# Kernel tuning notes

Measured on AMD Instinct MI355X. Metric: run time of the kernel, lower is better.

## Reference

```python
import jax, jax.numpy as jnp
import numpy as np

K = 8
HID = 32
BOUND = 5.0
SIGMA_MIN = 1e-4
MIN_DERIV = 1e-3
B, T, C = 32, 4096, 512


def setup_inputs() -> dict:
    key = jax.random.key(0)
    k1, k2, k3 = jax.random.split(key, 3)
    x = jax.random.normal(k1, (B, T, C), jnp.float32)
    W1 = jax.random.normal(k2, (HID, 2), jnp.float32) * 0.5
    b1 = jnp.zeros((HID,), jnp.float32)
    W2 = jax.random.normal(k3, (3 * K + 1, HID), jnp.float32) * 0.1
    b2 = jnp.zeros((3 * K + 1,), jnp.float32)
    return {"x": x, "W1": W1, "b1": b1, "W2": W2, "b2": b2}


def _rqs_forward(x2d, kx, ky, d):
    # x2d: (BC, T); kx, ky, d: (BC, K+1)
    w = kx[:, 1:] - kx[:, :-1]
    h = ky[:, 1:] - ky[:, :-1]
    s = h / jnp.maximum(w, 1e-8)
    idx = jax.vmap(lambda a, v: jnp.searchsorted(a, v, side='right'))(kx, x2d) - 1
    idx = jnp.clip(idx, 0, K - 1)  # (BC, T)
    g = lambda t, i: jnp.take_along_axis(t, i, axis=1)
    w_k = g(w, idx)
    h_k = g(h, idx)
    s_k = g(s, idx)
    d_k = g(d, idx)
    d_k1 = g(d, jnp.minimum(idx + 1, K))
    kx_l = g(kx, idx)
    ky_l = g(ky, idx)
    zeta = jnp.clip((x2d - kx_l) / jnp.maximum(w_k, 1e-8), 0.0, 1.0)
    numer = h_k * (s_k * zeta * zeta + d_k * zeta * (1.0 - zeta))
    denom = s_k + (d_k1 + d_k - 2.0 * s_k) * zeta * (1.0 - zeta)
    z2d = ky_l + numer / jnp.maximum(denom, 1e-8)
    tail = (x2d < -BOUND) | (x2d > BOUND)
    return jnp.where(tail, x2d, z2d)


def reference(x, W1, b1, W2, b2):
    Bb, Tt, Cc = x.shape
    # affine standardisation (unbiased std matching torch.std default)
    mu = jnp.mean(x, axis=1, keepdims=True)
    sig = jnp.maximum(jnp.std(x, axis=1, ddof=1, keepdims=True), SIGMA_MIN)
    z_pre = (x - mu) / sig  # (B, T, C)
    zd = jax.lax.stop_gradient(z_pre)
    skew = jnp.mean(zd ** 3, axis=1)          # (B, C)
    ekurt = jnp.mean(zd ** 4, axis=1) - 3.0   # (B, C)
    stats = jnp.stack([skew, ekurt], axis=-1).reshape(Bb * Cc, 2)
    hid = jax.nn.relu(stats @ W1.T + b1)
    raw = hid @ W2.T + b2                      # (BC, 3K+1)
    widths = jax.nn.softmax(raw[:, :K], axis=-1) * (2.0 * BOUND)
    heights = jax.nn.softmax(raw[:, K:2 * K], axis=-1) * (2.0 * BOUND)
    derivs = jax.nn.softplus(raw[:, 2 * K:]) + MIN_DERIV  # (BC, K+1)
    pad = jnp.full((widths.shape[0], 1), -BOUND, widths.dtype)
    kx = jnp.concatenate([pad, -BOUND + jnp.cumsum(widths, axis=-1)], axis=-1)
    ky = jnp.concatenate([pad, -BOUND + jnp.cumsum(heights, axis=-1)], axis=-1)
    x2d = jnp.transpose(z_pre, (0, 2, 1)).reshape(Bb * Cc, Tt)
    z2d = _rqs_forward(x2d, kx, ky, derivs)
    return jnp.transpose(z2d.reshape(Bb, Cc, Tt), (0, 2, 1))
```

## Files before the change

### kernel.cpp

```cpp
#include <hip/hip_runtime.h>
#include <math.h>

#define KNOTS 8
#define HIDN 32
#define TT 4096
#define CC 512
#define NB 32
#define BOUNDF 5.0f
#define CT 32
#define NTG 64
#define NLD 64
#define NPAIR 128
#define TPAD 9

typedef float f32x4 __attribute__((ext_vector_type(4)));

__global__ __launch_bounds__(512, 2)
void k_fused(const float* __restrict__ x, const float* __restrict__ W1,
             const float* __restrict__ b1, const float* __restrict__ W2,
             const float* __restrict__ b2, float* __restrict__ out)
{
    const int bb = blockIdx.y;
    const int c0 = blockIdx.x * CT;
    const int lc = threadIdx.x & 7;
    const int tg = threadIdx.x >> 3;

    __shared__ float red[NTG][4][CT];
    __shared__ float mom[4][CT];
    __shared__ float pA[CT], pB[CT];
    __shared__ float pKx[7][CT];
    __shared__ float2 bZ4[4][KNOTS][TPAD];
    __shared__ float2 bY4[4][KNOTS][TPAD];
    __shared__ float2 bD4[4][KNOTS][TPAD];

    const size_t base = (size_t)bb * TT * CC + c0 + 4 * lc + (size_t)tg * CC;
    const f32x4* pxt = (const f32x4*)(x + base);

    unsigned int xp[NPAIR];
    float s1[4] = {0,0,0,0}, s2[4] = {0,0,0,0}, s3[4] = {0,0,0,0}, s4[4] = {0,0,0,0};
    #pragma unroll
    for (int k = 0; k < NLD; ++k) {
        const f32x4 v = pxt[(size_t)k * (NTG * CC / 4)];
        #pragma unroll
        for (int q = 0; q < 4; ++q) {
            const float vv = v[q];
            const float v2 = vv * vv;
            s1[q] += vv;
            s2[q] = fmaf(vv, vv, s2[q]);
            s3[q] = fmaf(v2, vv, s3[q]);
            s4[q] = fmaf(v2, v2, s4[q]);
        }
        unsigned int pk0, pk1;
        asm("v_cvt_pk_bf16_f32 %0, %1, %2" : "=v"(pk0) : "v"(v[0]), "v"(v[1]));
        asm("v_cvt_pk_bf16_f32 %0, %1, %2" : "=v"(pk1) : "v"(v[2]), "v"(v[3]));
        xp[2*k]   = pk0;
        xp[2*k+1] = pk1;
    }
    #pragma unroll
    for (int q = 0; q < 4; ++q) {
        red[tg][0][4*lc+q] = s1[q];
        red[tg][1][4*lc+q] = s2[q];
        red[tg][2][4*lc+q] = s3[q];
        red[tg][3][4*lc+q] = s4[q];
    }
    __syncthreads();

    if (threadIdx.x < 4 * CT) {
        const int m = threadIdx.x >> 5, c = threadIdx.x & (CT - 1);
        float acc = 0.f;
        #pragma unroll
        for (int g = 0; g < NTG; ++g) acc += red[g][m][c];
        mom[m][c] = acc;
    }
    __syncthreads();

    if (threadIdx.x < CT) {
        const int c = threadIdx.x;
        const float n  = (float)TT;
        const float t1 = mom[0][c], t2 = mom[1][c], t3 = mom[2][c], t4 = mom[3][c];
        const float mu  = t1 / n;
        const float ex2 = t2 / n, ex3 = t3 / n, ex4 = t4 / n;
        float var = (t2 - n * mu * mu) / (n - 1.f);
        var = fmaxf(var, 0.f);
        const float sig  = fmaxf(sqrtf(var), 1e-4f);
        const float inv  = 1.f / sig;
        const float mu2  = mu * mu;
        const float ez3  = ex3 - 3.f * mu * ex2 + 2.f * mu * mu2;
        const float ez4  = ex4 - 4.f * mu * ex3 + 6.f * mu2 * ex2 - 3.f * mu2 * mu2;
        const float inv2 = inv * inv;
        const float skew  = ez3 * inv2 * inv;
        const float ekurt = ez4 * inv2 * inv2 - 3.f;

        float hid[HIDN];
        #pragma unroll
        for (int h = 0; h < HIDN; ++h) {
            float v = fmaf(W1[2*h], skew, fmaf(W1[2*h+1], ekurt, b1[h]));
            hid[h] = fmaxf(v, 0.f);
        }

        float e[KNOTS], kxr[KNOTS+1], kyr[KNOTS+1], dr[KNOTS+1];
        {
            float mx = -1e30f;
            #pragma unroll
            for (int o = 0; o < KNOTS; ++o) {
                float acc = b2[o];
                #pragma unroll
                for (int h = 0; h < HIDN; ++h) acc = fmaf(W2[o*HIDN + h], hid[h], acc);
                e[o] = acc; mx = fmaxf(mx, acc);
            }
            float sum = 0.f;
            #pragma unroll
            for (int o = 0; o < KNOTS; ++o) { e[o] = expf(e[o] - mx); sum += e[o]; }
            const float scale = (2.f * BOUNDF) / sum;
            float cum = -BOUNDF; kxr[0] = -BOUNDF;
            #pragma unroll
            for (int o = 0; o < KNOTS; ++o) { cum = fmaf(e[o], scale, cum); kxr[o+1] = cum; }
        }
        {
            float mx = -1e30f;
            #pragma unroll
            for (int o = 0; o < KNOTS; ++o) {
                float acc = b2[KNOTS + o];
                #pragma unroll
                for (int h = 0; h < HIDN; ++h) acc = fmaf(W2[(KNOTS+o)*HIDN + h], hid[h], acc);
                e[o] = acc; mx = fmaxf(mx, acc);
            }
            float sum = 0.f;
            #pragma unroll
            for (int o = 0; o < KNOTS; ++o) { e[o] = expf(e[o] - mx); sum += e[o]; }
            const float scale = (2.f * BOUNDF) / sum;
            float cum = -BOUNDF; kyr[0] = -BOUNDF;
            #pragma unroll
            for (int o = 0; o < KNOTS; ++o) { cum = fmaf(e[o], scale, cum); kyr[o+1] = cum; }
        }
        #pragma unroll
        for (int o = 0; o < KNOTS+1; ++o) {
            float acc = b2[2*KNOTS + o];
            #pragma unroll
            for (int h = 0; h < HIDN; ++h) acc = fmaf(W2[(2*KNOTS+o)*HIDN + h], hid[h], acc);
            float sp = fmaxf(acc, 0.f) + log1pf(expf(-fabsf(acc)));
            dr[o] = sp + 1e-3f;
        }

        pA[c] = inv;
        pB[c] = -mu * inv;
        #pragma unroll
        for (int j = 1; j <= 7; ++j) pKx[j-1][c] = kxr[j];
        const int q = c & 3, cc = c >> 2;
        #pragma unroll
        for (int j = 0; j < KNOTS; ++j) {
            const float w    = kxr[j+1] - kxr[j];
            const float wm   = fmaxf(w, 1e-8f);
            const float invw = 1.f / wm;
            const float h    = kyr[j+1] - kyr[j];
            bZ4[q][j][cc] = make_float2(-kxr[j] * invw, invw);
            bY4[q][j][cc] = make_float2(kyr[j], h);
            bD4[q][j][cc] = make_float2(dr[j], dr[j] + dr[j+1]);
        }
    }
    __syncthreads();

    float aq[4], bq[4], kx[4][7];
    #pragma unroll
    for (int q = 0; q < 4; ++q) {
        const int c = 4*lc + q;
        aq[q] = pA[c];
        bq[q] = pB[c];
        #pragma unroll
        for (int j = 0; j < 7; ++j) kx[q][j] = pKx[j][c];
    }
    f32x4* pot = (f32x4*)(out + base);

    #pragma unroll
    for (int k = 0; k < NLD; ++k) {
        const unsigned int u0 = xp[2*k], u1 = xp[2*k+1];
        float xv[4];
        xv[0] = __uint_as_float(u0 << 16);
        xv[1] = __uint_as_float(u0 & 0xffff0000u);
        xv[2] = __uint_as_float(u1 << 16);
        xv[3] = __uint_as_float(u1 & 0xffff0000u);
        f32x4 r;
        #pragma unroll
        for (int q = 0; q < 4; ++q) {
            const float z = fmaf(xv[q], aq[q], bq[q]);
            const bool  c4 = z >= kx[q][3];
            const float mB = c4 ? kx[q][5] : kx[q][1];
            const bool  cB = z >= mB;
            const float nLo = c4 ? kx[q][4] : kx[q][0];
            const float nHi = c4 ? kx[q][6] : kx[q][2];
            const float mC = cB ? nHi : nLo;
            const bool  cC = z >= mC;
            const int idx = (c4 ? 4 : 0) + (cB ? 2 : 0) + (cC ? 1 : 0);

            const float2 Z = bZ4[q][idx][lc];
            const float2 Y = bY4[q][idx][lc];
            const float2 D = bD4[q][idx][lc];

            const float zeta = fmaf(z, Z.y, Z.x);
            const float uu   = fmaf(-zeta, zeta, zeta);
            const float s    = Y.y * Z.y;
            const float R    = fmaf(-2.f, s, D.y);
            const float den  = fmaf(R, uu, s);
            const float inner= fmaf(s * zeta, zeta, D.x * uu);
            const float res  = fmaf(Y.y * inner,
                                    __builtin_amdgcn_rcpf(fmaxf(den, 1e-8f)), Y.x);
            r[q] = (fabsf(z) > BOUNDF) ? z : res;
        }
        __builtin_nontemporal_store(r, &pot[(size_t)k * (NTG * CC / 4)]);
    }
}

extern "C" void kernel_launch(void* const* d_in, const int* in_sizes, int n_in,
                              void* d_out, int out_size, void* d_ws, size_t ws_size,
                              hipStream_t stream) {
    const float* x  = (const float*)d_in[0];
    const float* W1 = (const float*)d_in[1];
    const float* b1 = (const float*)d_in[2];
    const float* W2 = (const float*)d_in[3];
    const float* b2 = (const float*)d_in[4];
    float* out = (float*)d_out;

    k_fused<<<dim3(CC / CT, NB), dim3(512), 0, stream>>>(x, W1, b1, W2, b2, out);
}
```

Baseline: 120.2 us.

## Split fused kernel into stats and apply kernels with workspace parameter tiles

Splits the single fused kernel into a statistics kernel that computes moments and spline parameters into a global workspace, and an apply kernel that re-reads x from memory. This removes the bf16 register cache of x and the register pressure that limited occupancy, and adds more parallelism in the apply phase. In exchange it reads the input twice from global memory and adds a second launch. The stats reduction also moves to wave shuffles.

```diff
diff --git a/kernel.cpp b/kernel.cpp
--- a/kernel.cpp
+++ b/kernel.cpp
@@ -7,74 +7,78 @@
 #define CC 512
 #define NB 32
 #define BOUNDF 5.0f
-#define CT 32
-#define NTG 64
-#define NLD 64
-#define NPAIR 128
-#define TPAD 9
+
+#define BZOFF 288
+#define BYOFF 1344
+#define BDOFF 2400
+#define TILEF 3456
 
 typedef float f32x4 __attribute__((ext_vector_type(4)));
 
-__global__ __launch_bounds__(512, 2)
-void k_fused(const float* __restrict__ x, const float* __restrict__ W1,
+__global__ __launch_bounds__(1024, 4)
+void k_stats(const float* __restrict__ x, const float* __restrict__ W1,
              const float* __restrict__ b1, const float* __restrict__ W2,
-             const float* __restrict__ b2, float* __restrict__ out)
+             const float* __restrict__ b2, float* __restrict__ ws)
 {
     const int bb = blockIdx.y;
-    const int c0 = blockIdx.x * CT;
+    const int ctile = blockIdx.x;
+    const int c0 = ctile * 32;
     const int lc = threadIdx.x & 7;
     const int tg = threadIdx.x >> 3;
-
-    __shared__ float red[NTG][4][CT];
-    __shared__ float mom[4][CT];
-    __shared__ float pA[CT], pB[CT];
-    __shared__ float pKx[7][CT];
-    __shared__ float2 bZ4[4][KNOTS][TPAD];
-    __shared__ float2 bY4[4][KNOTS][TPAD];
-    __shared__ float2 bD4[4][KNOTS][TPAD];
-
-    const size_t base = (size_t)bb * TT * CC + c0 + 4 * lc + (size_t)tg * CC;
-    const f32x4* pxt = (const f32x4*)(x + base);
-
-    unsigned int xp[NPAIR];
+    const int w  = threadIdx.x >> 6;
+    const int ln = threadIdx.x & 63;
+
+    __shared__ float red4[16][4][32];
+    __shared__ float mom[4][32];
+
+    const f32x4* pxt = (const f32x4*)(x + (size_t)bb * TT * CC + c0 + 4 * lc
+                                        + (size_t)tg * CC);
+    const size_t stride4 = (size_t)128 * CC / 4;
+
     float s1[4] = {0,0,0,0}, s2[4] = {0,0,0,0}, s3[4] = {0,0,0,0}, s4[4] = {0,0,0,0};
     #pragma unroll
-    for (int k = 0; k < NLD; ++k) {
-        const f32x4 v = pxt[(size_t)k * (NTG * CC / 4)];
-        #pragma unroll
-        for (int q = 0; q < 4; ++q) {
-            const float vv = v[q];
-            const float v2 = vv * vv;
+    for (int k = 0; k < 32; ++k) {
+        const f32x4 v = pxt[(size_t)k * stride4];
+        #pragma unroll
+        for (int q = 0; q < 4; ++q) {
+            const float vv = v[q], v2 = vv * vv;
             s1[q] += vv;
             s2[q] = fmaf(vv, vv, s2[q]);
             s3[q] = fmaf(v2, vv, s3[q]);
             s4[q] = fmaf(v2, v2, s4[q]);
         }
-        unsigned int pk0, pk1;
-        asm("v_cvt_pk_bf16_f32 %0, %1, %2" : "=v"(pk0) : "v"(v[0]), "v"(v[1]));
-        asm("v_cvt_pk_bf16_f32 %0, %1, %2" : "=v"(pk1) : "v"(v[2]), "v"(v[3]));
-        xp[2*k]   = pk0;
-        xp[2*k+1] = pk1;
     }
     #pragma unroll
-    for (int q = 0; q < 4; ++q) {
-        red[tg][0][4*lc+q] = s1[q];
-        red[tg][1][4*lc+q] = s2[q];
-        red[tg][2][4*lc+q] = s3[q];
-        red[tg][3][4*lc+q] = s4[q];
+    for (int m = 8; m < 64; m <<= 1) {
+        #pragma unroll
+        for (int q = 0; q < 4; ++q) {
+            s1[q] += __shfl_xor(s1[q], m, 64);
+            s2[q] += __shfl_xor(s2[q], m, 64);
+            s3[q] += __shfl_xor(s3[q], m, 64);
+            s4[q] += __shfl_xor(s4[q], m, 64);
+        }
+    }
+    if (ln < 8) {
+        #pragma unroll
+        for (int q = 0; q < 4; ++q) {
+            red4[w][0][4*ln+q] = s1[q];
+            red4[w][1][4*ln+q] = s2[q];
+            red4[w][2][4*ln+q] = s3[q];
+            red4[w][3][4*ln+q] = s4[q];
+        }
     }
     __syncthreads();
 
-    if (threadIdx.x < 4 * CT) {
-        const int m = threadIdx.x >> 5, c = threadIdx.x & (CT - 1);
+    if (threadIdx.x < 128) {
+        const int m = threadIdx.x >> 5, c = threadIdx.x & 31;
         float acc = 0.f;
         #pragma unroll
-        for (int g = 0; g < NTG; ++g) acc += red[g][m][c];
+        for (int g = 0; g < 16; ++g) acc += red4[g][m][c];
         mom[m][c] = acc;
     }
     __syncthreads();
 
-    if (threadIdx.x < CT) {
+    if (threadIdx.x < 32) {
         const int c = threadIdx.x;
         const float n  = (float)TT;
         const float t1 = mom[0][c], t2 = mom[1][c], t3 = mom[2][c], t4 = mom[3][c];
@@ -142,21 +146,43 @@
             dr[o] = sp + 1e-3f;
         }
 
-        pA[c] = inv;
-        pB[c] = -mu * inv;
-        #pragma unroll
-        for (int j = 1; j <= 7; ++j) pKx[j-1][c] = kxr[j];
-        const int q = c & 3, cc = c >> 2;
+        float* tb = ws + (size_t)(bb * 16 + ctile) * TILEF;
+        tb[c]      = inv;
+        tb[32 + c] = -mu * inv;
+        #pragma unroll
+        for (int j = 1; j <= 7; ++j) tb[64 + (j-1)*32 + c] = kxr[j];
+        float2* bz = (float2*)(tb + BZOFF);
+        float2* by = (float2*)(tb + BYOFF);
+        float2* bd = (float2*)(tb + BDOFF);
         #pragma unroll
         for (int j = 0; j < KNOTS; ++j) {
-            const float w    = kxr[j+1] - kxr[j];
-            const float wm   = fmaxf(w, 1e-8f);
+            const float wd   = kxr[j+1] - kxr[j];
+            const float wm   = fmaxf(wd, 1e-8f);
             const float invw = 1.f / wm;
             const float h    = kyr[j+1] - kyr[j];
-            bZ4[q][j][cc] = make_float2(-kxr[j] * invw, invw);
-            bY4[q][j][cc] = make_float2(kyr[j], h);
-            bD4[q][j][cc] = make_float2(dr[j], dr[j] + dr[j+1]);
-        }
+            bz[j*33 + c] = make_float2(-kxr[j] * invw, invw);
+            by[j*33 + c] = make_float2(kyr[j], h);
+            bd[j*33 + c] = make_float2(dr[j], dr[j] + dr[j+1]);
+        }
+    }
+}
+
+__global__ __launch_bounds__(256, 6)
+void k_apply(const float* __restrict__ x, const float* __restrict__ ws,
+             float* __restrict__ out)
+{
+    const int tch   = blockIdx.x;
+    const int ctile = blockIdx.y;
+    const int bb    = blockIdx.z;
+    const int c0 = ctile * 32;
+    const int lc = threadIdx.x & 7;
+    const int tg = threadIdx.x >> 3;
+
+    __shared__ float sp[TILEF];
+    {
+        const f32x4* src = (const f32x4*)(ws + (size_t)(bb * 16 + ctile) * TILEF);
+        f32x4* dst = (f32x4*)sp;
+        for (int i = threadIdx.x; i < TILEF / 4; i += 256) dst[i] = src[i];
     }
     __syncthreads();
 
@@ -164,25 +190,28 @@
     #pragma unroll
     for (int q = 0; q < 4; ++q) {
         const int c = 4*lc + q;
-        aq[q] = pA[c];
-        bq[q] = pB[c];
-        #pragma unroll
-        for (int j = 0; j < 7; ++j) kx[q][j] = pKx[j][c];
-    }
-    f32x4* pot = (f32x4*)(out + base);
-
-    #pragma unroll
-    for (int k = 0; k < NLD; ++k) {
-        const unsigned int u0 = xp[2*k], u1 = xp[2*k+1];
-        float xv[4];
-        xv[0] = __uint_as_float(u0 << 16);
-        xv[1] = __uint_as_float(u0 & 0xffff0000u);
-        xv[2] = __uint_as_float(u1 << 16);
-        xv[3] = __uint_as_float(u1 & 0xffff0000u);
+        aq[q] = sp[c];
+        bq[q] = sp[32 + c];
+        #pragma unroll
+        for (int j = 0; j < 7; ++j) kx[q][j] = sp[64 + j*32 + c];
+    }
+    const float2* bz = (const float2*)(sp + BZOFF);
+    const float2* by = (const float2*)(sp + BYOFF);
+    const float2* bd = (const float2*)(sp + BDOFF);
+
+    const size_t base = (size_t)bb * TT * CC + (size_t)(tch * 512 + tg) * CC
+                        + c0 + 4 * lc;
+    const f32x4* pxt = (const f32x4*)(x + base);
+    f32x4*       pot = (f32x4*)(out + base);
+    const size_t stride4 = (size_t)32 * CC / 4;
+
+    #pragma unroll 4
+    for (int k = 0; k < 16; ++k) {
+        const f32x4 v = pxt[(size_t)k * stride4];
         f32x4 r;
         #pragma unroll
         for (int q = 0; q < 4; ++q) {
-            const float z = fmaf(xv[q], aq[q], bq[q]);
+            const float z = fmaf(v[q], aq[q], bq[q]);
             const bool  c4 = z >= kx[q][3];
             const float mB = c4 ? kx[q][5] : kx[q][1];
             const bool  cB = z >= mB;
@@ -191,10 +220,11 @@
             const float mC = cB ? nHi : nLo;
             const bool  cC = z >= mC;
             const int idx = (c4 ? 4 : 0) + (cB ? 2 : 0) + (cC ? 1 : 0);
-
-            const float2 Z = bZ4[q][idx][lc];
-            const float2 Y = bY4[q][idx][lc];
-            const float2 D = bD4[q][idx][lc];
+            const int off = idx * 33 + 4*lc + q;
+
+            const float2 Z = bz[off];
+            const float2 Y = by[off];
+            const float2 D = bd[off];
 
             const float zeta = fmaf(z, Z.y, Z.x);
             const float uu   = fmaf(-zeta, zeta, zeta);
@@ -206,7 +236,7 @@
                                     __builtin_amdgcn_rcpf(fmaxf(den, 1e-8f)), Y.x);
             r[q] = (fabsf(z) > BOUNDF) ? z : res;
         }
-        __builtin_nontemporal_store(r, &pot[(size_t)k * (NTG * CC / 4)]);
+        __builtin_nontemporal_store(r, &pot[(size_t)k * stride4]);
     }
 }
 
@@ -219,6 +249,8 @@
     const float* W2 = (const float*)d_in[3];
     const float* b2 = (const float*)d_in[4];
     float* out = (float*)d_out;
-
-    k_fused<<<dim3(CC / CT, NB), dim3(512), 0, stream>>>(x, W1, b1, W2, b2, out);
+    float* ws  = (float*)d_ws;
+
+    k_stats<<<dim3(16, NB), dim3(1024), 0, stream>>>(x, W1, b1, W2, b2, ws);
+    k_apply<<<dim3(8, 16, NB), dim3(256), 0, stream>>>(x, ws, out);
 }
```

Result: slower. 156.0 us (+29.8%).

## Process two channel tiles per block, overlapping second tile's loads with first tile's stores

Applied to the files above, without the earlier changes.

Each block now handles 64 channels as two 32-channel tiles. While the transform of tile A runs and its results are stored, the loads and moment accumulation for tile B happen in the same loop, so load and store traffic overlap. The per-channel moment reduction also moves from a 64-row shared-memory table to wave-level shuffle reductions plus a small 8-row table. The cost is half as many blocks (256 instead of 512), which may reduce occupancy and latency hiding across the GPU, and a serial finalize phase between the tiles.

```diff
diff --git a/kernel.cpp b/kernel.cpp
--- a/kernel.cpp
+++ b/kernel.cpp
@@ -7,13 +7,98 @@
 #define CC 512
 #define NB 32
 #define BOUNDF 5.0f
-#define CT 32
-#define NTG 64
 #define NLD 64
-#define NPAIR 128
-#define TPAD 9
+#define TPAD 33
 
 typedef float f32x4 __attribute__((ext_vector_type(4)));
+
+__device__ __forceinline__ void finalize_ch(
+    int c, float t1, float t2, float t3, float t4,
+    const float* __restrict__ W1, const float* __restrict__ b1,
+    const float* __restrict__ W2, const float* __restrict__ b2,
+    float* pA, float* pB, float* pKx ,
+    float2* bz, float2* by, float2* bd )
+{
+    const float n  = (float)TT;
+    const float mu  = t1 / n;
+    const float ex2 = t2 / n, ex3 = t3 / n, ex4 = t4 / n;
+    float var = (t2 - n * mu * mu) / (n - 1.f);
+    var = fmaxf(var, 0.f);
+    const float sig  = fmaxf(sqrtf(var), 1e-4f);
+    const float inv  = 1.f / sig;
+    const float mu2  = mu * mu;
+    const float ez3  = ex3 - 3.f * mu * ex2 + 2.f * mu * mu2;
+    const float ez4  = ex4 - 4.f * mu * ex3 + 6.f * mu2 * ex2 - 3.f * mu2 * mu2;
+    const float inv2 = inv * inv;
+    const float skew  = ez3 * inv2 * inv;
+    const float ekurt = ez4 * inv2 * inv2 - 3.f;
+
+    float hid[HIDN];
+    #pragma unroll
+    for (int h = 0; h < HIDN; ++h) {
+        float v = fmaf(W1[2*h], skew, fmaf(W1[2*h+1], ekurt, b1[h]));
+        hid[h] = fmaxf(v, 0.f);
+    }
+
+    float e[KNOTS], kxr[KNOTS+1], kyr[KNOTS+1], dr[KNOTS+1];
+    {
+        float mx = -1e30f;
+        #pragma unroll
+        for (int o = 0; o < KNOTS; ++o) {
+            float acc = b2[o];
+            #pragma unroll
+            for (int h = 0; h < HIDN; ++h) acc = fmaf(W2[o*HIDN + h], hid[h], acc);
+            e[o] = acc; mx = fmaxf(mx, acc);
+        }
+        float sum = 0.f;
+        #pragma unroll
+        for (int o = 0; o < KNOTS; ++o) { e[o] = expf(e[o] - mx); sum += e[o]; }
+        const float scale = (2.f * BOUNDF) / sum;
+        float cum = -BOUNDF; kxr[0] = -BOUNDF;
+        #pragma unroll
+        for (int o = 0; o < KNOTS; ++o) { cum = fmaf(e[o], scale, cum); kxr[o+1] = cum; }
+    }
+    {
+        float mx = -1e30f;
+        #pragma unroll
+        for (int o = 0; o < KNOTS; ++o) {
+            float acc = b2[KNOTS + o];
+            #pragma unroll
+            for (int h = 0; h < HIDN; ++h) acc = fmaf(W2[(KNOTS+o)*HIDN + h], hid[h], acc);
+            e[o] = acc; mx = fmaxf(mx, acc);
+        }
+        float sum = 0.f;
+        #pragma unroll
+        for (int o = 0; o < KNOTS; ++o) { e[o] = expf(e[o] - mx); sum += e[o]; }
+        const float scale = (2.f * BOUNDF) / sum;
+        float cum = -BOUNDF; kyr[0] = -BOUNDF;
+        #pragma unroll
+        for (int o = 0; o < KNOTS; ++o) { cum = fmaf(e[o], scale, cum); kyr[o+1] = cum; }
+    }
+    #pragma unroll
+    for (int o = 0; o < KNOTS+1; ++o) {
+        float acc = b2[2*KNOTS + o];
+        #pragma unroll
+        for (int h = 0; h < HIDN; ++h) acc = fmaf(W2[(2*KNOTS+o)*HIDN + h], hid[h], acc);
+        float sp = fmaxf(acc, 0.f) + log1pf(expf(-fabsf(acc)));
+        dr[o] = sp + 1e-3f;
+    }
+
+    pA[c] = inv;
+    pB[c] = -mu * inv;
+    #pragma unroll
+    for (int j = 1; j <= 7; ++j) pKx[(j-1)*32 + c] = kxr[j];
+    #pragma unroll
+    for (int j = 0; j < KNOTS; ++j) {
+        const float wd   = kxr[j+1] - kxr[j];
+        const float wm   = fmaxf(wd, 1e-8f);
+        const float invw = 1.f / wm;
+        const float h    = kyr[j+1] - kyr[j];
+        bz[j*TPAD + c] = make_float2(-kxr[j] * invw, invw);
+        by[j*TPAD + c] = make_float2(kyr[j], h);
+        bd[j*TPAD + c] = make_float2(dr[j], dr[j] + dr[j+1]);
+    }
+}
 
 __global__ __launch_bounds__(512, 2)
 void k_fused(const float* __restrict__ x, const float* __restrict__ W1,
@@ -21,30 +106,34 @@
              const float* __restrict__ b2, float* __restrict__ out)
 {
     const int bb = blockIdx.y;
-    const int c0 = blockIdx.x * CT;
+    const int jj = blockIdx.x;
+    const int c0a = jj * 64;
     const int lc = threadIdx.x & 7;
     const int tg = threadIdx.x >> 3;
-
-    __shared__ float red[NTG][4][CT];
-    __shared__ float mom[4][CT];
-    __shared__ float pA[CT], pB[CT];
-    __shared__ float pKx[7][CT];
-    __shared__ float2 bZ4[4][KNOTS][TPAD];
-    __shared__ float2 bY4[4][KNOTS][TPAD];
-    __shared__ float2 bD4[4][KNOTS][TPAD];
-
-    const size_t base = (size_t)bb * TT * CC + c0 + 4 * lc + (size_t)tg * CC;
-    const f32x4* pxt = (const f32x4*)(x + base);
-
-    unsigned int xp[NPAIR];
+    const int w  = threadIdx.x >> 6;
+    const int ln = threadIdx.x & 63;
+
+    __shared__ float red4[8][4][32];
+    __shared__ float mom[4][32];
+    __shared__ float pA[2][32], pB[2][32], pKx[2][7*32];
+    __shared__ float2 bzT[2][KNOTS*TPAD], byT[2][KNOTS*TPAD], bdT[2][KNOTS*TPAD];
+
+    const size_t baseA = (size_t)bb * TT * CC + c0a + 4 * lc + (size_t)tg * CC;
+    const f32x4* pxA = (const f32x4*)(x + baseA);
+    const f32x4* pxB = (const f32x4*)(x + baseA + 32);
+    f32x4* poA = (f32x4*)(out + baseA);
+    f32x4* poB = (f32x4*)(out + baseA + 32);
+    const size_t stride4 = (size_t)64 * CC / 4;
+
+    unsigned int xp[2 * NLD];
     float s1[4] = {0,0,0,0}, s2[4] = {0,0,0,0}, s3[4] = {0,0,0,0}, s4[4] = {0,0,0,0};
+
     #pragma unroll
     for (int k = 0; k < NLD; ++k) {
-        const f32x4 v = pxt[(size_t)k * (NTG * CC / 4)];
-        #pragma unroll
-        for (int q = 0; q < 4; ++q) {
-            const float vv = v[q];
-            const float v2 = vv * vv;
+        const f32x4 v = pxA[(size_t)k * stride4];
+        #pragma unroll
+        for (int q = 0; q < 4; ++q) {
+            const float vv = v[q], v2 = vv * vv;
             s1[q] += vv;
             s2[q] = fmaf(vv, vv, s2[q]);
             s3[q] = fmaf(v2, vv, s3[q]);
@@ -53,123 +142,145 @@
         unsigned int pk0, pk1;
         asm("v_cvt_pk_bf16_f32 %0, %1, %2" : "=v"(pk0) : "v"(v[0]), "v"(v[1]));
         asm("v_cvt_pk_bf16_f32 %0, %1, %2" : "=v"(pk1) : "v"(v[2]), "v"(v[3]));
-        xp[2*k]   = pk0;
-        xp[2*k+1] = pk1;
-    }
-    #pragma unroll
-    for (int q = 0; q < 4; ++q) {
-        red[tg][0][4*lc+q] = s1[q];
-        red[tg][1][4*lc+q] = s2[q];
-        red[tg][2][4*lc+q] = s3[q];
-        red[tg][3][4*lc+q] = s4[q];
-    }
-    __syncthreads();
-
-    if (threadIdx.x < 4 * CT) {
-        const int m = threadIdx.x >> 5, c = threadIdx.x & (CT - 1);
+        xp[2*k] = pk0; xp[2*k+1] = pk1;
+    }
+    #pragma unroll
+    for (int m = 8; m < 64; m <<= 1)
+        #pragma unroll
+        for (int q = 0; q < 4; ++q) {
+            s1[q] += __shfl_xor(s1[q], m, 64);
+            s2[q] += __shfl_xor(s2[q], m, 64);
+            s3[q] += __shfl_xor(s3[q], m, 64);
+            s4[q] += __shfl_xor(s4[q], m, 64);
+        }
+    if (ln < 8) {
+        #pragma unroll
+        for (int q = 0; q < 4; ++q) {
+            red4[w][0][4*ln+q] = s1[q];
+            red4[w][1][4*ln+q] = s2[q];
+            red4[w][2][4*ln+q] = s3[q];
+            red4[w][3][4*ln+q] = s4[q];
+        }
+    }
+    __syncthreads();
+    if (threadIdx.x < 128) {
+        const int m = threadIdx.x >> 5, c = threadIdx.x & 31;
         float acc = 0.f;
         #pragma unroll
-        for (int g = 0; g < NTG; ++g) acc += red[g][m][c];
+        for (int g = 0; g < 8; ++g) acc += red4[g][m][c];
         mom[m][c] = acc;
     }
     __syncthreads();
-
-    if (threadIdx.x < CT) {
-        const int c = threadIdx.x;
-        const float n  = (float)TT;
-        const float t1 = mom[0][c], t2 = mom[1][c], t3 = mom[2][c], t4 = mom[3][c];
-        const float mu  = t1 / n;
-        const float ex2 = t2 / n, ex3 = t3 / n, ex4 = t4 / n;
-        float var = (t2 - n * mu * mu) / (n - 1.f);
-        var = fmaxf(var, 0.f);
-        const float sig  = fmaxf(sqrtf(var), 1e-4f);
-        const float inv  = 1.f / sig;
-        const float mu2  = mu * mu;
-        const float ez3  = ex3 - 3.f * mu * ex2 + 2.f * mu * mu2;
-        const float ez4  = ex4 - 4.f * mu * ex3 + 6.f * mu2 * ex2 - 3.f * mu2 * mu2;
-        const float inv2 = inv * inv;
-        const float skew  = ez3 * inv2 * inv;
-        const float ekurt = ez4 * inv2 * inv2 - 3.f;
-
-        float hid[HIDN];
-        #pragma unroll
-        for (int h = 0; h < HIDN; ++h) {
-            float v = fmaf(W1[2*h], skew, fmaf(W1[2*h+1], ekurt, b1[h]));
-            hid[h] = fmaxf(v, 0.f);
-        }
-
-        float e[KNOTS], kxr[KNOTS+1], kyr[KNOTS+1], dr[KNOTS+1];
-        {
-            float mx = -1e30f;
-            #pragma unroll
-            for (int o = 0; o < KNOTS; ++o) {
-                float acc = b2[o];
-                #pragma unroll
-                for (int h = 0; h < HIDN; ++h) acc = fmaf(W2[o*HIDN + h], hid[h], acc);
-                e[o] = acc; mx = fmaxf(mx, acc);
-            }
-            float sum = 0.f;
-            #pragma unroll
-            for (int o = 0; o < KNOTS; ++o) { e[o] = expf(e[o] - mx); sum += e[o]; }
-            const float scale = (2.f * BOUNDF) / sum;
-            float cum = -BOUNDF; kxr[0] = -BOUNDF;
-            #pragma unroll
-            for (int o = 0; o < KNOTS; ++o) { cum = fmaf(e[o], scale, cum); kxr[o+1] = cum; }
-        }
-        {
-            float mx = -1e30f;
-            #pragma unroll
-            for (int o = 0; o < KNOTS; ++o) {
-                float acc = b2[KNOTS + o];
-                #pragma unroll
-                for (int h = 0; h < HIDN; ++h) acc = fmaf(W2[(KNOTS+o)*HIDN + h], hid[h], acc);
-                e[o] = acc; mx = fmaxf(mx, acc);
-            }
-            float sum = 0.f;
-            #pragma unroll
-            for (int o = 0; o < KNOTS; ++o) { e[o] = expf(e[o] - mx); sum += e[o]; }
-            const float scale = (2.f * BOUNDF) / sum;
-            float cum = -BOUNDF; kyr[0] = -BOUNDF;
-            #pragma unroll
-            for (int o = 0; o < KNOTS; ++o) { cum = fmaf(e[o], scale, cum); kyr[o+1] = cum; }
-        }
-        #pragma unroll
-        for (int o = 0; o < KNOTS+1; ++o) {
-            float acc = b2[2*KNOTS + o];
-            #pragma unroll
-            for (int h = 0; h < HIDN; ++h) acc = fmaf(W2[(2*KNOTS+o)*HIDN + h], hid[h], acc);
-            float sp = fmaxf(acc, 0.f) + log1pf(expf(-fabsf(acc)));
-            dr[o] = sp + 1e-3f;
-        }
-
-        pA[c] = inv;
-        pB[c] = -mu * inv;
-        #pragma unroll
-        for (int j = 1; j <= 7; ++j) pKx[j-1][c] = kxr[j];
-        const int q = c & 3, cc = c >> 2;
-        #pragma unroll
-        for (int j = 0; j < KNOTS; ++j) {
-            const float w    = kxr[j+1] - kxr[j];
-            const float wm   = fmaxf(w, 1e-8f);
-            const float invw = 1.f / wm;
-            const float h    = kyr[j+1] - kyr[j];
-            bZ4[q][j][cc] = make_float2(-kxr[j] * invw, invw);
-            bY4[q][j][cc] = make_float2(kyr[j], h);
-            bD4[q][j][cc] = make_float2(dr[j], dr[j] + dr[j+1]);
-        }
-    }
-    __syncthreads();
-
-    float aq[4], bq[4], kx[4][7];
+    if (threadIdx.x < 32)
+        finalize_ch(threadIdx.x, mom[0][threadIdx.x], mom[1][threadIdx.x],
+                    mom[2][threadIdx.x], mom[3][threadIdx.x],
+                    W1, b1, W2, b2, pA[0], pB[0], pKx[0], bzT[0], byT[0], bdT[0]);
+    __syncthreads();
+
+    float aq[4], bq[4], kxq[4][7];
     #pragma unroll
     for (int q = 0; q < 4; ++q) {
         const int c = 4*lc + q;
-        aq[q] = pA[c];
-        bq[q] = pB[c];
-        #pragma unroll
-        for (int j = 0; j < 7; ++j) kx[q][j] = pKx[j][c];
-    }
-    f32x4* pot = (f32x4*)(out + base);
+        aq[q] = pA[0][c]; bq[q] = pB[0][c];
+        #pragma unroll
+        for (int j = 0; j < 7; ++j) kxq[q][j] = pKx[0][j*32 + c];
+    }
+
+    #pragma unroll
+    for (int q = 0; q < 4; ++q) { s1[q]=0.f; s2[q]=0.f; s3[q]=0.f; s4[q]=0.f; }
+    #pragma unroll
+    for (int k = 0; k < NLD; ++k) {
+        {
+            const unsigned int u0 = xp[2*k], u1 = xp[2*k+1];
+            float xv[4];
+            xv[0] = __uint_as_float(u0 << 16);
+            xv[1] = __uint_as_float(u0 & 0xffff0000u);
+            xv[2] = __uint_as_float(u1 << 16);
+            xv[3] = __uint_as_float(u1 & 0xffff0000u);
+            f32x4 r;
+            #pragma unroll
+            for (int q = 0; q < 4; ++q) {
+                const float z = fmaf(xv[q], aq[q], bq[q]);
+                const bool  c4 = z >= kxq[q][3];
+                const float mB = c4 ? kxq[q][5] : kxq[q][1];
+                const bool  cB = z >= mB;
+                const float nLo = c4 ? kxq[q][4] : kxq[q][0];
+                const float nHi = c4 ? kxq[q][6] : kxq[q][2];
+                const float mC = cB ? nHi : nLo;
+                const bool  cC = z >= mC;
+                const int idx = (c4 ? 4 : 0) + (cB ? 2 : 0) + (cC ? 1 : 0);
+                const int off = idx * TPAD + 4*lc + q;
+                const float2 Z = bzT[0][off];
+                const float2 Y = byT[0][off];
+                const float2 D = bdT[0][off];
+                const float zeta = fmaf(z, Z.y, Z.x);
+                const float uu   = fmaf(-zeta, zeta, zeta);
+                const float s    = Y.y * Z.y;
+                const float R    = fmaf(-2.f, s, D.y);
+                const float den  = fmaf(R, uu, s);
+                const float inner= fmaf(s * zeta, zeta, D.x * uu);
+                const float res  = fmaf(Y.y * inner,
+                                        __builtin_amdgcn_rcpf(fmaxf(den, 1e-8f)), Y.x);
+                r[q] = (fabsf(z) > BOUNDF) ? z : res;
+            }
+            __builtin_nontemporal_store(r, &poA[(size_t)k * stride4]);
+        }
+        {
+            const f32x4 v = pxB[(size_t)k * stride4];
+            #pragma unroll
+            for (int q = 0; q < 4; ++q) {
+                const float vv = v[q], v2 = vv * vv;
+                s1[q] += vv;
+                s2[q] = fmaf(vv, vv, s2[q]);
+                s3[q] = fmaf(v2, vv, s3[q]);
+                s4[q] = fmaf(v2, v2, s4[q]);
+            }
+            unsigned int pk0, pk1;
+            asm("v_cvt_pk_bf16_f32 %0, %1, %2" : "=v"(pk0) : "v"(v[0]), "v"(v[1]));
+            asm("v_cvt_pk_bf16_f32 %0, %1, %2" : "=v"(pk1) : "v"(v[2]), "v"(v[3]));
+            xp[2*k] = pk0; xp[2*k+1] = pk1;
+        }
+    }
+    #pragma unroll
+    for (int m = 8; m < 64; m <<= 1)
+        #pragma unroll
+        for (int q = 0; q < 4; ++q) {
+            s1[q] += __shfl_xor(s1[q], m, 64);
+            s2[q] += __shfl_xor(s2[q], m, 64);
+            s3[q] += __shfl_xor(s3[q], m, 64);
+            s4[q] += __shfl_xor(s4[q], m, 64);
+        }
+    if (ln < 8) {
+        #pragma unroll
+        for (int q = 0; q < 4; ++q) {
+            red4[w][0][4*ln+q] = s1[q];
+            red4[w][1][4*ln+q] = s2[q];
+            red4[w][2][4*ln+q] = s3[q];
+            red4[w][3][4*ln+q] = s4[q];
+        }
+    }
+    __syncthreads();
+    if (threadIdx.x < 128) {
+        const int m = threadIdx.x >> 5, c = threadIdx.x & 31;
+        float acc = 0.f;
+        #pragma unroll
+        for (int g = 0; g < 8; ++g) acc += red4[g][m][c];
+        mom[m][c] = acc;
+    }
+    __syncthreads();
+    if (threadIdx.x < 32)
+        finalize_ch(threadIdx.x, mom[0][threadIdx.x], mom[1][threadIdx.x],
+                    mom[2][threadIdx.x], mom[3][threadIdx.x],
+                    W1, b1, W2, b2, pA[1], pB[1], pKx[1], bzT[1], byT[1], bdT[1]);
+    __syncthreads();
+
+    #pragma unroll
+    for (int q = 0; q < 4; ++q) {
+        const int c = 4*lc + q;
+        aq[q] = pA[1][c]; bq[q] = pB[1][c];
+        #pragma unroll
+        for (int j = 0; j < 7; ++j) kxq[q][j] = pKx[1][j*32 + c];
+    }
 
     #pragma unroll
     for (int k = 0; k < NLD; ++k) {
@@ -183,19 +294,18 @@
         #pragma unroll
         for (int q = 0; q < 4; ++q) {
             const float z = fmaf(xv[q], aq[q], bq[q]);
-            const bool  c4 = z >= kx[q][3];
-            const float mB = c4 ? kx[q][5] : kx[q][1];
+            const bool  c4 = z >= kxq[q][3];
+            const float mB = c4 ? kxq[q][5] : kxq[q][1];
             const bool  cB = z >= mB;
-            const float nLo = c4 ? kx[q][4] : kx[q][0];
-            const float nHi = c4 ? kx[q][6] : kx[q][2];
+            const float nLo = c4 ? kxq[q][4] : kxq[q][0];
+            const float nHi = c4 ? kxq[q][6] : kxq[q][2];
             const float mC = cB ? nHi : nLo;
             const bool  cC = z >= mC;
             const int idx = (c4 ? 4 : 0) + (cB ? 2 : 0) + (cC ? 1 : 0);
-
-            const float2 Z = bZ4[q][idx][lc];
-            const float2 Y = bY4[q][idx][lc];
-            const float2 D = bD4[q][idx][lc];
-
+            const int off = idx * TPAD + 4*lc + q;
+            const float2 Z = bzT[1][off];
+            const float2 Y = byT[1][off];
+            const float2 D = bdT[1][off];
             const float zeta = fmaf(z, Z.y, Z.x);
             const float uu   = fmaf(-zeta, zeta, zeta);
             const float s    = Y.y * Z.y;
@@ -206,7 +316,7 @@
                                     __builtin_amdgcn_rcpf(fmaxf(den, 1e-8f)), Y.x);
             r[q] = (fabsf(z) > BOUNDF) ? z : res;
         }
-        __builtin_nontemporal_store(r, &pot[(size_t)k * (NTG * CC / 4)]);
+        __builtin_nontemporal_store(r, &poB[(size_t)k * stride4]);
     }
 }
 
@@ -220,5 +330,5 @@
     const float* b2 = (const float*)d_in[4];
     float* out = (float*)d_out;
 
-    k_fused<<<dim3(CC / CT, NB), dim3(512), 0, stream>>>(x, W1, b1, W2, b2, out);
+    k_fused<<<dim3(8, NB), dim3(512), 0, stream>>>(x, W1, b1, W2, b2, out);
 }
```

After: 121.5 us. About the same (+1.0%).
